# Optimization experiments

Measured on AMD Instinct MI355X. Metric: run time of the kernel, lower is better.

## Reference

```python
import jax, jax.numpy as jnp
import numpy as np

MAX_DISP = 40
STRIDE_2 = 1
EPS = 1e-06  # hardcoded in the torch module's CosineSimilarity


def setup_inputs() -> dict:
    key = jax.random.key(0)
    k1, k2 = jax.random.split(key)
    B, C, H, W = 4, 256, 128, 256
    x_1 = jax.random.normal(k1, (B, C, H, W), dtype=jnp.float32)
    x_2 = jax.random.normal(k2, (B, C, H, W), dtype=jnp.float32)
    return {"x_1": x_1, "x_2": x_2}


def reference(x_1, x_2):
    B, C, H, W = x_1.shape
    # pad x_2 on the right of the width axis by max_disp (zeros)
    x2p = jnp.pad(x_2, ((0, 0), (0, 0), (0, 0), (0, MAX_DISP)))
    # channel L2 norms computed ONCE (the fusion opportunity)
    n1 = jnp.sqrt(jnp.sum(x_1 * x_1, axis=1))            # [B, H, W]
    n2p = jnp.sqrt(jnp.sum(x2p * x2p, axis=1))           # [B, H, W+D]
    sims = []
    for d in range(0, MAX_DISP + 1, STRIDE_2):           # fixed small set of 41 shifts
        x2s = jax.lax.dynamic_slice_in_dim(x2p, d, W, axis=3)   # [B, C, H, W]
        n2 = jax.lax.dynamic_slice_in_dim(n2p, d, W, axis=2)    # [B, H, W]
        dot = jnp.einsum('bchw,bchw->bhw', x_1, x2s)
        sims.append(dot / jnp.maximum(n1 * n2, EPS))
    return jnp.stack(sims, axis=1)                       # [B, 41, H, W]
```

## Files before the change

### kernel.cpp

```cpp
#include <hip/hip_runtime.h>
#include <hip/hip_bf16.h>


#define B_   4
#define C_   256
#define H_   128
#define W_   256
#define ND_  41
#define HW_  (H_ * W_)
#define CHW_ (C_ * HW_)
#define EPS_ 1e-6f

typedef __attribute__((ext_vector_type(4))) float f32x4;
typedef __attribute__((ext_vector_type(8))) short bf16x8;

#define ABASE 0
#define BBASE 20480
#define NBASE 44800
#define LDSZ  47040

__device__ __forceinline__ unsigned bfr(float x) {
  unsigned u = __builtin_bit_cast(unsigned, x);
  return (u + 0x7fffu + ((u >> 16) & 1u)) >> 16;
}

__global__ __launch_bounds__(512, 4)
void corr_mfma(const float* __restrict__ x1, const float* __restrict__ x2,
               float* __restrict__ out) {
  __shared__ __align__(16) char lds[LDSZ];

  const int tid = threadIdx.x;
  const int l   = tid & 63;
  const int v   = tid >> 6;
  const int m   = l & 15;
  const int g   = l >> 4;

  const int r = blockIdx.x;
  const int b = r >> 7;
  const int h = r & (H_ - 1);

  const float* X1 = x1 + b * CHW_ + h * W_;
  const float* X2 = x2 + b * CHW_ + h * W_;

  if (tid < 560) ((float*)(lds + NBASE))[tid] = 0.f;
  {
    unsigned* zp = (unsigned*)(lds + BBASE + 256 * 80);
    zp[tid] = 0u;
    if (tid < 960 - 512) zp[tid + 512] = 0u;
  }

  int wadr1[4];
#pragma unroll
  for (int j = 0; j < 4; ++j) {
    int w = 4 * l + j;
    wadr1[j] = ABASE + w * 80 + (((v >> 1) + w) % 5) * 16 + (v & 1) * 8;
  }
  int adrA[2], adrB[2][4];
#pragma unroll
  for (int i = 0; i < 2; ++i) {
    int wt = v + 8 * i;
    int rowA = 16 * wt + m;
    adrA[i] = ABASE + rowA * 80 + ((g + rowA) % 5) * 16;
#pragma unroll
    for (int c = 0; c < 4; ++c) {
      int col = 16 * (wt + c) + m;
      adrB[i][c] = BBASE + col * 80 + ((g + col) % 5) * 16;
    }
  }

  f32x4 acc[2][4];
#pragma unroll
  for (int i = 0; i < 2; ++i)
#pragma unroll
    for (int c = 0; c < 4; ++c) acc[i][c] = (f32x4){0.f, 0.f, 0.f, 0.f};

  float ssq1[4] = {0.f, 0.f, 0.f, 0.f}, ssq2[4] = {0.f, 0.f, 0.f, 0.f};

  f32x4 r1[4], r2[4];
#pragma unroll
  for (int i = 0; i < 4; ++i) {
    r1[i] = *(const f32x4*)(X1 + (4 * v + i) * HW_ + 4 * l);
    r2[i] = *(const f32x4*)(X2 + (4 * v + i) * HW_ + 4 * l);
  }

  for (int ks = 0; ks < 8; ++ks) {
    __syncthreads();
#pragma unroll
    for (int j = 0; j < 4; ++j) {
#pragma unroll
      for (int i = 0; i < 4; ++i) {
        ssq1[j] += r1[i][j] * r1[i][j];
        ssq2[j] += r2[i][j] * r2[i][j];
      }
      uint2 p1, p2;
      p1.x = bfr(r1[0][j]) | (bfr(r1[1][j]) << 16);
      p1.y = bfr(r1[2][j]) | (bfr(r1[3][j]) << 16);
      p2.x = bfr(r2[0][j]) | (bfr(r2[1][j]) << 16);
      p2.y = bfr(r2[2][j]) | (bfr(r2[3][j]) << 16);
      *(uint2*)(lds + wadr1[j]) = p1;
      *(uint2*)(lds + wadr1[j] + (BBASE - ABASE)) = p2;
    }
    __syncthreads();
    if (ks < 7) {
      const float* p1 = X1 + ((ks + 1) * 32 + 4 * v) * HW_ + 4 * l;
      const float* p2 = X2 + ((ks + 1) * 32 + 4 * v) * HW_ + 4 * l;
#pragma unroll
      for (int i = 0; i < 4; ++i) {
        r1[i] = *(const f32x4*)(p1 + i * HW_);
        r2[i] = *(const f32x4*)(p2 + i * HW_);
      }
    }
    bf16x8 a0 = *(const bf16x8*)(lds + adrA[0]);
    bf16x8 a1 = *(const bf16x8*)(lds + adrA[1]);
#pragma unroll
    for (int c = 0; c < 4; ++c) {
      bf16x8 b0 = *(const bf16x8*)(lds + adrB[0][c]);
      acc[0][c] = __builtin_amdgcn_mfma_f32_16x16x32_bf16(a0, b0, acc[0][c], 0, 0, 0);
    }
#pragma unroll
    for (int c = 0; c < 4; ++c) {
      bf16x8 b1 = *(const bf16x8*)(lds + adrB[1][c]);
      acc[1][c] = __builtin_amdgcn_mfma_f32_16x16x32_bf16(a1, b1, acc[1][c], 0, 0, 0);
    }
  }

  float* nsq = (float*)(lds + NBASE);
#pragma unroll
  for (int j = 0; j < 4; ++j) {
    atomicAdd(nsq + 4 * l + j, ssq1[j]);
    atomicAdd(nsq + 256 + 4 * l + j, ssq2[j]);
  }
  __syncthreads();
  if (tid < 256) nsq[tid] = sqrtf(nsq[tid]);
  else           nsq[tid] = sqrtf(nsq[tid]);
  if (tid < 48)  nsq[512 + tid] = sqrtf(nsq[512 + tid]);
  __syncthreads();

  float* Sw  = (float*)(lds + v * 4224);
  float* n1s = nsq;
  float* n2s = nsq + 256;
  const int wq = l & 3, dd = l >> 2;
#pragma unroll
  for (int i = 0; i < 2; ++i) {
    int wt = v + 8 * i;
#pragma unroll
    for (int c = 0; c < 4; ++c)
#pragma unroll
      for (int rr = 0; rr < 4; ++rr)
        Sw[(4 * g + rr) * 66 + 16 * c + m] = acc[i][c][rr];
#pragma unroll
    for (int p = 0; p < 3; ++p) {
      int d  = 16 * p + dd;
      int w0 = 16 * wt + 4 * wq;
      f32x4 o;
#pragma unroll
      for (int j = 0; j < 4; ++j) {
        int mm = 4 * wq + j;
        float dot = Sw[mm * 66 + mm + d];
        o[j] = dot / fmaxf(n1s[w0 + j] * n2s[w0 + j + d], EPS_);
      }
      if (d <= 40)
        *(f32x4*)(out + ((b * ND_ + d) * H_ + h) * W_ + w0) = o;
    }
  }
}

extern "C" void kernel_launch(void* const* d_in, const int* in_sizes, int n_in,
                              void* d_out, int out_size, void* d_ws, size_t ws_size,
                              hipStream_t stream) {
  const float* x1 = (const float*)d_in[0];
  const float* x2 = (const float*)d_in[1];
  float* out = (float*)d_out;
  dim3 grid(B_ * H_);
  dim3 block(512);
  hipLaunchKernelGGL(corr_mfma, grid, block, 0, stream, x1, x2, out);
}
```

Measured before the change: 61.98 us.

## Double block size to 1024 threads, one output tile per wave

Each row block now launches 16 waves instead of 8. Every wave owns a single 16-wide output tile and loads 2 channels per K step instead of 4. The aim is more memory-level parallelism and fewer registers per thread, since each thread now holds half the accumulators and staging registers. In exchange, LDS per block grows to about 70KB to hold the larger per-wave scratch area. The tight launch bound also risks register spilling or limiting how many blocks fit on a CU.

```diff
diff --git a/kernel.cpp b/kernel.cpp
--- a/kernel.cpp
+++ b/kernel.cpp
@@ -16,15 +16,15 @@
 
 #define ABASE 0
 #define BBASE 20480
-#define NBASE 44800
-#define LDSZ  47040
+#define NBASE 67584
+#define LDSZ  69824
 
 __device__ __forceinline__ unsigned bfr(float x) {
   unsigned u = __builtin_bit_cast(unsigned, x);
   return (u + 0x7fffu + ((u >> 16) & 1u)) >> 16;
 }
 
-__global__ __launch_bounds__(512, 4)
+__global__ __launch_bounds__(1024, 8)
 void corr_mfma(const float* __restrict__ x1, const float* __restrict__ x2,
                float* __restrict__ out) {
   __shared__ __align__(16) char lds[LDSZ];
@@ -43,84 +43,61 @@
   const float* X2 = x2 + b * CHW_ + h * W_;
 
   if (tid < 560) ((float*)(lds + NBASE))[tid] = 0.f;
-  {
-    unsigned* zp = (unsigned*)(lds + BBASE + 256 * 80);
-    zp[tid] = 0u;
-    if (tid < 960 - 512) zp[tid + 512] = 0u;
-  }
+  if (tid < 960) ((unsigned*)(lds + BBASE + 256 * 80))[tid] = 0u;
 
-  int wadr1[4];
+  int wadr[4];
 #pragma unroll
   for (int j = 0; j < 4; ++j) {
     int w = 4 * l + j;
-    wadr1[j] = ABASE + w * 80 + (((v >> 1) + w) % 5) * 16 + (v & 1) * 8;
+    wadr[j] = ABASE + w * 80 + (((v >> 2) + w) % 5) * 16 + (v & 3) * 4;
   }
-  int adrA[2], adrB[2][4];
+  const int rowA = 16 * v + m;
+  const int adrA = ABASE + rowA * 80 + ((g + rowA) % 5) * 16;
+  int adrB[4];
+#pragma unroll
+  for (int c = 0; c < 4; ++c) {
+    int col = 16 * (v + c) + m;
+    adrB[c] = BBASE + col * 80 + ((g + col) % 5) * 16;
+  }
+
+  f32x4 acc[4];
+#pragma unroll
+  for (int c = 0; c < 4; ++c) acc[c] = (f32x4){0.f, 0.f, 0.f, 0.f};
+  float ssq1[4] = {0.f, 0.f, 0.f, 0.f}, ssq2[4] = {0.f, 0.f, 0.f, 0.f};
+
+  f32x4 r1[2], r2[2];
 #pragma unroll
   for (int i = 0; i < 2; ++i) {
-    int wt = v + 8 * i;
-    int rowA = 16 * wt + m;
-    adrA[i] = ABASE + rowA * 80 + ((g + rowA) % 5) * 16;
-#pragma unroll
-    for (int c = 0; c < 4; ++c) {
-      int col = 16 * (wt + c) + m;
-      adrB[i][c] = BBASE + col * 80 + ((g + col) % 5) * 16;
-    }
-  }
-
-  f32x4 acc[2][4];
-#pragma unroll
-  for (int i = 0; i < 2; ++i)
-#pragma unroll
-    for (int c = 0; c < 4; ++c) acc[i][c] = (f32x4){0.f, 0.f, 0.f, 0.f};
-
-  float ssq1[4] = {0.f, 0.f, 0.f, 0.f}, ssq2[4] = {0.f, 0.f, 0.f, 0.f};
-
-  f32x4 r1[4], r2[4];
-#pragma unroll
-  for (int i = 0; i < 4; ++i) {
-    r1[i] = *(const f32x4*)(X1 + (4 * v + i) * HW_ + 4 * l);
-    r2[i] = *(const f32x4*)(X2 + (4 * v + i) * HW_ + 4 * l);
+    r1[i] = *(const f32x4*)(X1 + (2 * v + i) * HW_ + 4 * l);
+    r2[i] = *(const f32x4*)(X2 + (2 * v + i) * HW_ + 4 * l);
   }
 
   for (int ks = 0; ks < 8; ++ks) {
     __syncthreads();
 #pragma unroll
     for (int j = 0; j < 4; ++j) {
-#pragma unroll
-      for (int i = 0; i < 4; ++i) {
-        ssq1[j] += r1[i][j] * r1[i][j];
-        ssq2[j] += r2[i][j] * r2[i][j];
-      }
-      uint2 p1, p2;
-      p1.x = bfr(r1[0][j]) | (bfr(r1[1][j]) << 16);
-      p1.y = bfr(r1[2][j]) | (bfr(r1[3][j]) << 16);
-      p2.x = bfr(r2[0][j]) | (bfr(r2[1][j]) << 16);
-      p2.y = bfr(r2[2][j]) | (bfr(r2[3][j]) << 16);
-      *(uint2*)(lds + wadr1[j]) = p1;
-      *(uint2*)(lds + wadr1[j] + (BBASE - ABASE)) = p2;
+      ssq1[j] += r1[0][j] * r1[0][j] + r1[1][j] * r1[1][j];
+      ssq2[j] += r2[0][j] * r2[0][j] + r2[1][j] * r2[1][j];
+      unsigned p1 = bfr(r1[0][j]) | (bfr(r1[1][j]) << 16);
+      unsigned p2 = bfr(r2[0][j]) | (bfr(r2[1][j]) << 16);
+      *(unsigned*)(lds + wadr[j]) = p1;
+      *(unsigned*)(lds + wadr[j] + BBASE) = p2;
     }
     __syncthreads();
     if (ks < 7) {
-      const float* p1 = X1 + ((ks + 1) * 32 + 4 * v) * HW_ + 4 * l;
-      const float* p2 = X2 + ((ks + 1) * 32 + 4 * v) * HW_ + 4 * l;
+      const float* p1 = X1 + ((ks + 1) * 32 + 2 * v) * HW_ + 4 * l;
+      const float* p2 = X2 + ((ks + 1) * 32 + 2 * v) * HW_ + 4 * l;
 #pragma unroll
-      for (int i = 0; i < 4; ++i) {
+      for (int i = 0; i < 2; ++i) {
         r1[i] = *(const f32x4*)(p1 + i * HW_);
         r2[i] = *(const f32x4*)(p2 + i * HW_);
       }
     }
-    bf16x8 a0 = *(const bf16x8*)(lds + adrA[0]);
-    bf16x8 a1 = *(const bf16x8*)(lds + adrA[1]);
+    bf16x8 a0 = *(const bf16x8*)(lds + adrA);
 #pragma unroll
     for (int c = 0; c < 4; ++c) {
-      bf16x8 b0 = *(const bf16x8*)(lds + adrB[0][c]);
-      acc[0][c] = __builtin_amdgcn_mfma_f32_16x16x32_bf16(a0, b0, acc[0][c], 0, 0, 0);
-    }
-#pragma unroll
-    for (int c = 0; c < 4; ++c) {
-      bf16x8 b1 = *(const bf16x8*)(lds + adrB[1][c]);
-      acc[1][c] = __builtin_amdgcn_mfma_f32_16x16x32_bf16(a1, b1, acc[1][c], 0, 0, 0);
+      bf16x8 b0 = *(const bf16x8*)(lds + adrB[c]);
+      acc[c] = __builtin_amdgcn_mfma_f32_16x16x32_bf16(a0, b0, acc[c], 0, 0, 0);
     }
   }
 
@@ -131,27 +108,23 @@
     atomicAdd(nsq + 256 + 4 * l + j, ssq2[j]);
   }
   __syncthreads();
-  if (tid < 256) nsq[tid] = sqrtf(nsq[tid]);
-  else           nsq[tid] = sqrtf(nsq[tid]);
-  if (tid < 48)  nsq[512 + tid] = sqrtf(nsq[512 + tid]);
+  if (tid < 560) nsq[tid] = sqrtf(nsq[tid]);
   __syncthreads();
 
   float* Sw  = (float*)(lds + v * 4224);
   float* n1s = nsq;
   float* n2s = nsq + 256;
+#pragma unroll
+  for (int c = 0; c < 4; ++c)
+#pragma unroll
+    for (int rr = 0; rr < 4; ++rr)
+      Sw[(4 * g + rr) * 66 + 16 * c + m] = acc[c][rr];
   const int wq = l & 3, dd = l >> 2;
+  const int w0 = 16 * v + 4 * wq;
 #pragma unroll
-  for (int i = 0; i < 2; ++i) {
-    int wt = v + 8 * i;
-#pragma unroll
-    for (int c = 0; c < 4; ++c)
-#pragma unroll
-      for (int rr = 0; rr < 4; ++rr)
-        Sw[(4 * g + rr) * 66 + 16 * c + m] = acc[i][c][rr];
-#pragma unroll
-    for (int p = 0; p < 3; ++p) {
-      int d  = 16 * p + dd;
-      int w0 = 16 * wt + 4 * wq;
+  for (int p = 0; p < 3; ++p) {
+    int d = 16 * p + dd;
+    if (d <= 40) {
       f32x4 o;
 #pragma unroll
       for (int j = 0; j < 4; ++j) {
@@ -159,8 +132,7 @@
         float dot = Sw[mm * 66 + mm + d];
         o[j] = dot / fmaxf(n1s[w0 + j] * n2s[w0 + j + d], EPS_);
       }
-      if (d <= 40)
-        *(f32x4*)(out + ((b * ND_ + d) * H_ + h) * W_ + w0) = o;
+      *(f32x4*)(out + ((b * ND_ + d) * H_ + h) * W_ + w0) = o;
     }
   }
 }
@@ -172,6 +144,6 @@
   const float* x2 = (const float*)d_in[1];
   float* out = (float*)d_out;
   dim3 grid(B_ * H_);
-  dim3 block(512);
+  dim3 block(1024);
   hipLaunchKernelGGL(corr_mfma, grid, block, 0, stream, x1, x2, out);
 }
```

Result: slower. 71.72 us (+15.7%).
